# Optimization experiments

Measured on AMD Instinct MI355X. Metric: run time of the kernel, lower is better.

## Reference

```python
import jax, jax.numpy as jnp
import numpy as np

B, T, Q, K, H = 32, 2048, 1024, 1024, 1024

def setup_inputs() -> dict:
    key = jax.random.key(0)
    k1, k2, k3, k4, k5, k6 = jax.random.split(key, 6)
    queries = jax.random.normal(k1, (B, 1, Q), dtype=jnp.float32)
    keys = jax.random.normal(k2, (B, T, K), dtype=jnp.float32)
    pad_mask = jax.random.randint(k3, (B, T, 1), 0, 2) == 1
    # Linear weights stored pre-transposed: x @ W computes nn.Linear(x)
    W_q = jax.random.normal(k4, (Q, H), dtype=jnp.float32) / np.sqrt(Q)
    W_k = jax.random.normal(k5, (K, H), dtype=jnp.float32) / np.sqrt(K)
    w_v = jax.random.normal(k6, (H, 1), dtype=jnp.float32) / np.sqrt(H)
    return {"queries": queries, "keys": keys, "pad_mask": pad_mask,
            "W_q": W_q, "W_k": W_k, "w_v": w_v}

def reference(queries, keys, pad_mask, W_q, W_k, w_v):
    trans_q = queries @ W_q                      # (B, 1, H)
    trans_k = keys @ W_k                         # (B, T, H)
    features = jnp.tanh(trans_q + trans_k)       # (B, T, H) broadcast add
    scores = features @ w_v                      # (B, T, 1)
    scores = jnp.where(pad_mask, -jnp.inf, scores)
    attn_weights = jax.nn.softmax(scores, axis=1)  # softmax over T (dropout p=0.0 is identity)
    # bmm(keys^T (B,K,T), attn (B,T,1)) -> (B, K, 1)
    context = jnp.einsum('btk,bto->bko', keys, attn_weights)
    return attn_weights, context
```

## Files before the change

### kernel.cpp

```cpp
#include <hip/hip_runtime.h>
#include <hip/hip_bf16.h>

#define NB 32
#define NT 2048
#define NH 1024

typedef __attribute__((ext_vector_type(4))) float f32x4;
typedef __attribute__((ext_vector_type(8))) __bf16 bf16x8;

__device__ __forceinline__ unsigned short f2bf(float f) {
  __bf16 h = (__bf16)f;
  return __builtin_bit_cast(unsigned short, h);
}

__device__ __forceinline__ float fast_tanh(float x) {
  float e = __expf(2.0f * x);
  return 1.0f - 2.0f / (e + 1.0f);
}

__device__ __forceinline__ void gload_lds16(const void* gptr, void* lptr) {
  auto g = reinterpret_cast<const __attribute__((address_space(1))) unsigned int*>(
      reinterpret_cast<uintptr_t>(gptr));
  auto l = reinterpret_cast<__attribute__((address_space(3))) unsigned int*>(
      reinterpret_cast<uintptr_t>(lptr));
  __builtin_amdgcn_global_load_lds(g, l, 16, 0, 0);
}

__global__ __launch_bounds__(256) void tq_kernel(
    const float* __restrict__ q, const float* __restrict__ Wq, float* __restrict__ tq) {
  __shared__ float qs[1024];
  int b = blockIdx.x >> 2;
  int h = ((blockIdx.x & 3) << 8) + threadIdx.x;
  f32x4 qv = *(const f32x4*)(q + b * 1024 + threadIdx.x * 4);
  *(f32x4*)(qs + threadIdx.x * 4) = qv;
  __syncthreads();
  float acc = 0.f;
  const float* wp = Wq + h;
#pragma unroll 8
  for (int k = 0; k < 1024; ++k) acc = fmaf(qs[k], wp[(size_t)k * 1024], acc);
  tq[b * 1024 + h] = acc;
}

__global__ __launch_bounds__(256) void wkt_kernel(
    const float* __restrict__ Wk, unsigned short* __restrict__ WkT) {
  __shared__ float tile[64][68];
  int kt = blockIdx.x & 15;
  int ht = blockIdx.x >> 4;
  int tid = threadIdx.x;
  int r = tid >> 4;
  int c = (tid & 15) * 4;
#pragma unroll
  for (int i = 0; i < 4; ++i) {
    int rr = i * 16 + r;
    f32x4 v = *(const f32x4*)(Wk + (size_t)(kt * 64 + rr) * 1024 + ht * 64 + c);
    tile[rr][c + 0] = v.x; tile[rr][c + 1] = v.y;
    tile[rr][c + 2] = v.z; tile[rr][c + 3] = v.w;
  }
  __syncthreads();
#pragma unroll
  for (int i = 0; i < 4; ++i) {
    int hh = i * 16 + r;
    ushort4 o;
    o.x = f2bf(tile[c + 0][hh]); o.y = f2bf(tile[c + 1][hh]);
    o.z = f2bf(tile[c + 2][hh]); o.w = f2bf(tile[c + 3][hh]);
    *(ushort4*)(WkT + (size_t)(ht * 64 + hh) * 1024 + kt * 64 + c) = o;
  }
}

__global__ __launch_bounds__(256, 2) void score_kernel(
    const float* __restrict__ keys, const unsigned short* __restrict__ WkT,
    const float* __restrict__ tq, const float* __restrict__ wv,
    float* __restrict__ scores) {
  __shared__ unsigned short As[2][128 * 64];
  __shared__ unsigned short Bs[2][128 * 64];

  const int bid = blockIdx.x;
  const int xcd = bid & 7;
  const int j = bid >> 3;
  const int m_strip = xcd * 64 + (j >> 3);
  const int h_tile = j & 7;
  const int row0 = m_strip * 128;
  const int col0 = h_tile * 128;
  const int b = row0 >> 11;

  const int tid = threadIdx.x;
  const int lane = tid & 63;
  const int w = tid >> 6;

  int a_r[4], a_ss[4], a_dst[4];
#pragma unroll
  for (int c = 0; c < 4; ++c) {
    int q = c * 256 + tid;
    int r = q >> 3, slot = q & 7;
    a_r[c] = r;
    a_ss[c] = slot ^ (r & 7);
    a_dst[c] = r * 64 + slot * 8;
  }

  f32x4 fa[4][2];

  auto A_issue = [&](int kt) {
#pragma unroll
    for (int c = 0; c < 4; ++c) {
      const float* src = keys + (size_t)(row0 + a_r[c]) * 1024 + kt * 64 + a_ss[c] * 8;
      fa[c][0] = *(const f32x4*)(src);
      fa[c][1] = *(const f32x4*)(src + 4);
    }
  };
  auto A_write = [&](int buf) {
#pragma unroll
    for (int c = 0; c < 4; ++c) {
      bf16x8 v;
#pragma unroll
      for (int e = 0; e < 4; ++e) {
        v[e] = (__bf16)fa[c][0][e];
        v[4 + e] = (__bf16)fa[c][1][e];
      }
      *(bf16x8*)(&As[buf][a_dst[c]]) = v;
    }
  };
  auto B_issue = [&](int kt, int buf) {
#pragma unroll
    for (int i = 0; i < 4; ++i) {
      int n = w * 32 + i * 8 + (lane >> 3);
      int ss = (lane & 7) ^ (n & 7);
      const unsigned short* g = WkT + (size_t)(col0 + n) * 1024 + kt * 64 + ss * 8;
      gload_lds16(g, &Bs[buf][(w * 32 + i * 8) * 64]);
    }
  };

  A_issue(0);
  B_issue(0, 0);
  A_write(0);
  __syncthreads();

  f32x4 acc[4][4];
#pragma unroll
  for (int m = 0; m < 4; ++m)
#pragma unroll
    for (int n = 0; n < 4; ++n) acc[m][n] = (f32x4){0.f, 0.f, 0.f, 0.f};

  const int m_half = (w >> 1) * 64;
  const int n_half = (w & 1) * 64;
  const int lrow = lane & 15;
  const int lk = lane >> 4;

#pragma unroll 2
  for (int kt = 0; kt < 16; ++kt) {
    int cur = kt & 1;
    if (kt < 15) {
      A_issue(kt + 1);
      B_issue(kt + 1, cur ^ 1);
    }
#pragma unroll
    for (int kk = 0; kk < 2; ++kk) {
      bf16x8 af[4], bfr[4];
#pragma unroll
      for (int m = 0; m < 4; ++m) {
        int r = m_half + m * 16 + lrow;
        int slot = (kk * 4 + lk) ^ (r & 7);
        af[m] = *(const bf16x8*)(&As[cur][r * 64 + slot * 8]);
      }
#pragma unroll
      for (int n = 0; n < 4; ++n) {
        int r = n_half + n * 16 + lrow;
        int slot = (kk * 4 + lk) ^ (r & 7);
        bfr[n] = *(const bf16x8*)(&Bs[cur][r * 64 + slot * 8]);
      }
#pragma unroll
      for (int m = 0; m < 4; ++m)
#pragma unroll
        for (int n = 0; n < 4; ++n)
          acc[m][n] = __builtin_amdgcn_mfma_f32_16x16x32_bf16(af[m], bfr[n], acc[m][n], 0, 0, 0);
    }
    if (kt < 15) A_write(cur ^ 1);
    __syncthreads();
  }

  float tql[4], wvl[4];
#pragma unroll
  for (int n = 0; n < 4; ++n) {
    int h = col0 + n_half + n * 16 + lrow;
    tql[n] = tq[b * 1024 + h];
    wvl[n] = wv[h];
  }
  float rs[4][4];
#pragma unroll
  for (int m = 0; m < 4; ++m)
#pragma unroll
    for (int jj = 0; jj < 4; ++jj) rs[m][jj] = 0.f;
#pragma unroll
  for (int m = 0; m < 4; ++m)
#pragma unroll
    for (int n = 0; n < 4; ++n)
#pragma unroll
      for (int jj = 0; jj < 4; ++jj)
        rs[m][jj] += fast_tanh(acc[m][n][jj] + tql[n]) * wvl[n];
#pragma unroll
  for (int m = 0; m < 4; ++m)
#pragma unroll
    for (int jj = 0; jj < 4; ++jj) {
      float v = rs[m][jj];
      v += __shfl_xor(v, 1);
      v += __shfl_xor(v, 2);
      v += __shfl_xor(v, 4);
      v += __shfl_xor(v, 8);
      rs[m][jj] = v;
    }
  if ((lane & 15) == 0) {
#pragma unroll
    for (int m = 0; m < 4; ++m)
#pragma unroll
      for (int jj = 0; jj < 4; ++jj)
        atomicAdd(&scores[row0 + m_half + m * 16 + lk * 4 + jj], rs[m][jj]);
  }
}

__global__ __launch_bounds__(256) void softmax_kernel(
    const float* __restrict__ scores, const int* __restrict__ mask,
    float* __restrict__ attn) {
  int b = blockIdx.x;
  int tid = threadIdx.x;
  int lane = tid & 63, wid = tid >> 6;
  __shared__ float red[4];
  float loc[8];
  float mx = -1e30f;
#pragma unroll
  for (int i = 0; i < 8; ++i) {
    int t = i * 256 + tid;
    float s = scores[b * 2048 + t];
    if (mask[b * 2048 + t] != 0) s = -INFINITY;
    loc[i] = s;
    mx = fmaxf(mx, s);
  }
#pragma unroll
  for (int d = 1; d < 64; d <<= 1) mx = fmaxf(mx, __shfl_xor(mx, d));
  if (lane == 0) red[wid] = mx;
  __syncthreads();
  mx = fmaxf(fmaxf(red[0], red[1]), fmaxf(red[2], red[3]));
  __syncthreads();
  float sum = 0.f;
#pragma unroll
  for (int i = 0; i < 8; ++i) {
    float e = __expf(loc[i] - mx);
    loc[i] = e;
    sum += e;
  }
#pragma unroll
  for (int d = 1; d < 64; d <<= 1) sum += __shfl_xor(sum, d);
  if (lane == 0) red[wid] = sum;
  __syncthreads();
  sum = red[0] + red[1] + red[2] + red[3];
  float inv = 1.f / sum;
#pragma unroll
  for (int i = 0; i < 8; ++i) attn[b * 2048 + i * 256 + tid] = loc[i] * inv;
}

__global__ __launch_bounds__(256) void context_kernel(
    const float* __restrict__ keys, const float* __restrict__ attn,
    float* __restrict__ ctx) {
  int bid = blockIdx.x;
  int b = bid >> 5, ts = bid & 31;
  int tid = threadIdx.x;
  const float* kp = keys + (size_t)b * 2048 * 1024 + (size_t)ts * 64 * 1024 + tid * 4;
  const float* ap = attn + b * 2048 + ts * 64;
  f32x4 acc = {0.f, 0.f, 0.f, 0.f};
#pragma unroll 4
  for (int i = 0; i < 64; ++i) {
    float wgt = ap[i];
    if (wgt != 0.f) {
      f32x4 kv = *(const f32x4*)(kp + (size_t)i * 1024);
      acc += kv * wgt;
    }
  }
  float* c = ctx + b * 1024 + tid * 4;
  atomicAdd(c + 0, acc[0]);
  atomicAdd(c + 1, acc[1]);
  atomicAdd(c + 2, acc[2]);
  atomicAdd(c + 3, acc[3]);
}

extern "C" void kernel_launch(void* const* d_in, const int* in_sizes, int n_in,
                              void* d_out, int out_size, void* d_ws, size_t ws_size,
                              hipStream_t stream) {
  const float* queries = (const float*)d_in[0];
  const float* keys    = (const float*)d_in[1];
  const int*   mask    = (const int*)d_in[2];
  const float* Wq      = (const float*)d_in[3];
  const float* Wk      = (const float*)d_in[4];
  const float* wv      = (const float*)d_in[5];

  float* out  = (float*)d_out;
  float* attn = out;
  float* ctx  = out + 65536;

  char* ws = (char*)d_ws;
  float* tq             = (float*)ws;
  float* scores         = (float*)(ws + 131072);
  unsigned short* WkT   = (unsigned short*)(ws + 131072 + 262144);

  hipMemsetAsync(scores, 0, 65536 * sizeof(float), stream);
  hipMemsetAsync(ctx, 0, 32768 * sizeof(float), stream);

  tq_kernel<<<128, 256, 0, stream>>>(queries, Wq, tq);
  wkt_kernel<<<256, 256, 0, stream>>>(Wk, WkT);
  score_kernel<<<4096, 256, 0, stream>>>(keys, WkT, tq, wv, scores);
  softmax_kernel<<<32, 256, 0, stream>>>(scores, mask, attn);
  context_kernel<<<1024, 256, 0, stream>>>(keys, attn, ctx);
}
```

Measured before the change: 682.5 us.

## Single-buffer score GEMM LDS for higher occupancy, split tq K, deterministic ctx reduce

The score GEMM drops from double-buffered to single-buffered LDS tiles and raises launch bounds from 2 to 4 blocks per CU. Global loads of A are prefetched two tiles ahead in registers, and an extra barrier per iteration keeps the shared buffer consistent. The tq kernel splits the K dimension across 4x more blocks and combines them with atomics. Context now writes per-chunk partials that a new reduction kernel sums instead of using atomics. The trade is more barriers and less overlap inside a block, in exchange for more resident waves to hide latency.

```diff
diff --git a/kernel.cpp b/kernel.cpp
--- a/kernel.cpp
+++ b/kernel.cpp
@@ -28,17 +28,19 @@
 
 __global__ __launch_bounds__(256) void tq_kernel(
     const float* __restrict__ q, const float* __restrict__ Wq, float* __restrict__ tq) {
-  __shared__ float qs[1024];
-  int b = blockIdx.x >> 2;
-  int h = ((blockIdx.x & 3) << 8) + threadIdx.x;
-  f32x4 qv = *(const f32x4*)(q + b * 1024 + threadIdx.x * 4);
-  *(f32x4*)(qs + threadIdx.x * 4) = qv;
+  __shared__ float qs[256];
+  int bx = blockIdx.x;
+  int b = bx >> 4, hc = (bx >> 2) & 3, ks = bx & 3;
+  int tid = threadIdx.x;
+  int h = hc * 256 + tid;
+  int k0 = ks * 256;
+  qs[tid] = q[b * 1024 + k0 + tid];
   __syncthreads();
   float acc = 0.f;
-  const float* wp = Wq + h;
+  const float* wp = Wq + (size_t)k0 * 1024 + h;
 #pragma unroll 8
-  for (int k = 0; k < 1024; ++k) acc = fmaf(qs[k], wp[(size_t)k * 1024], acc);
-  tq[b * 1024 + h] = acc;
+  for (int k = 0; k < 256; ++k) acc = fmaf(qs[k], wp[(size_t)k * 1024], acc);
+  atomicAdd(&tq[b * 1024 + h], acc);
 }
 
 __global__ __launch_bounds__(256) void wkt_kernel(
@@ -67,12 +69,12 @@
   }
 }
 
-__global__ __launch_bounds__(256, 2) void score_kernel(
+__global__ __launch_bounds__(256, 4) void score_kernel(
     const float* __restrict__ keys, const unsigned short* __restrict__ WkT,
     const float* __restrict__ tq, const float* __restrict__ wv,
     float* __restrict__ scores) {
-  __shared__ unsigned short As[2][128 * 64];
-  __shared__ unsigned short Bs[2][128 * 64];
+  __shared__ unsigned short As[128 * 64];
+  __shared__ unsigned short Bs[128 * 64];
 
   const int bid = blockIdx.x;
   const int xcd = bid & 7;
@@ -107,7 +109,7 @@
       fa[c][1] = *(const f32x4*)(src + 4);
     }
   };
-  auto A_write = [&](int buf) {
+  auto A_write = [&]() {
 #pragma unroll
     for (int c = 0; c < 4; ++c) {
       bf16x8 v;
@@ -116,22 +118,23 @@
         v[e] = (__bf16)fa[c][0][e];
         v[4 + e] = (__bf16)fa[c][1][e];
       }
-      *(bf16x8*)(&As[buf][a_dst[c]]) = v;
+      *(bf16x8*)(&As[a_dst[c]]) = v;
     }
   };
-  auto B_issue = [&](int kt, int buf) {
+  auto B_issue = [&](int kt) {
 #pragma unroll
     for (int i = 0; i < 4; ++i) {
       int n = w * 32 + i * 8 + (lane >> 3);
       int ss = (lane & 7) ^ (n & 7);
       const unsigned short* g = WkT + (size_t)(col0 + n) * 1024 + kt * 64 + ss * 8;
-      gload_lds16(g, &Bs[buf][(w * 32 + i * 8) * 64]);
+      gload_lds16(g, &Bs[(w * 32 + i * 8) * 64]);
     }
   };
 
   A_issue(0);
-  B_issue(0, 0);
-  A_write(0);
+  B_issue(0);
+  A_write();
+  A_issue(1);
   __syncthreads();
 
   f32x4 acc[4][4];
@@ -145,13 +148,7 @@
   const int lrow = lane & 15;
   const int lk = lane >> 4;
 
-#pragma unroll 2
   for (int kt = 0; kt < 16; ++kt) {
-    int cur = kt & 1;
-    if (kt < 15) {
-      A_issue(kt + 1);
-      B_issue(kt + 1, cur ^ 1);
-    }
 #pragma unroll
     for (int kk = 0; kk < 2; ++kk) {
       bf16x8 af[4], bfr[4];
@@ -159,13 +156,13 @@
       for (int m = 0; m < 4; ++m) {
         int r = m_half + m * 16 + lrow;
         int slot = (kk * 4 + lk) ^ (r & 7);
-        af[m] = *(const bf16x8*)(&As[cur][r * 64 + slot * 8]);
+        af[m] = *(const bf16x8*)(&As[r * 64 + slot * 8]);
       }
 #pragma unroll
       for (int n = 0; n < 4; ++n) {
         int r = n_half + n * 16 + lrow;
         int slot = (kk * 4 + lk) ^ (r & 7);
-        bfr[n] = *(const bf16x8*)(&Bs[cur][r * 64 + slot * 8]);
+        bfr[n] = *(const bf16x8*)(&Bs[r * 64 + slot * 8]);
       }
 #pragma unroll
       for (int m = 0; m < 4; ++m)
@@ -173,8 +170,13 @@
         for (int n = 0; n < 4; ++n)
           acc[m][n] = __builtin_amdgcn_mfma_f32_16x16x32_bf16(af[m], bfr[n], acc[m][n], 0, 0, 0);
     }
-    if (kt < 15) A_write(cur ^ 1);
     __syncthreads();
+    if (kt < 15) {
+      A_write();
+      B_issue(kt + 1);
+      if (kt < 14) A_issue(kt + 2);
+      __syncthreads();
+    }
   }
 
   float tql[4], wvl[4];
@@ -258,7 +260,7 @@
 
 __global__ __launch_bounds__(256) void context_kernel(
     const float* __restrict__ keys, const float* __restrict__ attn,
-    float* __restrict__ ctx) {
+    float* __restrict__ partial) {
   int bid = blockIdx.x;
   int b = bid >> 5, ts = bid & 31;
   int tid = threadIdx.x;
@@ -273,11 +275,17 @@
       acc += kv * wgt;
     }
   }
-  float* c = ctx + b * 1024 + tid * 4;
-  atomicAdd(c + 0, acc[0]);
-  atomicAdd(c + 1, acc[1]);
-  atomicAdd(c + 2, acc[2]);
-  atomicAdd(c + 3, acc[3]);
+  *(f32x4*)(partial + (size_t)(b * 32 + ts) * 1024 + tid * 4) = acc;
+}
+
+__global__ __launch_bounds__(256) void ctx_reduce_kernel(
+    const float* __restrict__ partial, float* __restrict__ ctx) {
+  int o = blockIdx.x * 256 + threadIdx.x;
+  int b = o >> 10, k = o & 1023;
+  float s = 0.f;
+#pragma unroll 8
+  for (int tc = 0; tc < 32; ++tc) s += partial[(size_t)(b * 32 + tc) * 1024 + k];
+  ctx[o] = s;
 }
 
 extern "C" void kernel_launch(void* const* d_in, const int* in_sizes, int n_in,
@@ -296,15 +304,17 @@
 
   char* ws = (char*)d_ws;
   float* tq             = (float*)ws;
-  float* scores         = (float*)(ws + 131072);
-  unsigned short* WkT   = (unsigned short*)(ws + 131072 + 262144);
-
+  float* scores         = (float*)(ws + (128 << 10));
+  unsigned short* WkT   = (unsigned short*)(ws + (384 << 10));
+  float* partial        = (float*)(ws + (384 << 10) + (2 << 20));
+
+  hipMemsetAsync(tq, 0, 32768 * sizeof(float), stream);
   hipMemsetAsync(scores, 0, 65536 * sizeof(float), stream);
-  hipMemsetAsync(ctx, 0, 32768 * sizeof(float), stream);
-
-  tq_kernel<<<128, 256, 0, stream>>>(queries, Wq, tq);
+
+  tq_kernel<<<512, 256, 0, stream>>>(queries, Wq, tq);
   wkt_kernel<<<256, 256, 0, stream>>>(Wk, WkT);
   score_kernel<<<4096, 256, 0, stream>>>(keys, WkT, tq, wv, scores);
   softmax_kernel<<<32, 256, 0, stream>>>(scores, mask, attn);
-  context_kernel<<<1024, 256, 0, stream>>>(keys, attn, ctx);
-}
+  context_kernel<<<1024, 256, 0, stream>>>(keys, attn, partial);
+  ctx_reduce_kernel<<<128, 256, 0, stream>>>(partial, ctx);
+}
```

Result: slower. 766.8 us (+12.3%).
